# Kernel tuning notes

Measured on AMD Instinct MI355X. Metric: run time of the kernel, lower is better.

Reference implementation:

```python
import jax, jax.numpy as jnp
import numpy as np

OUT, IN, RANK = 4096, 4096, 512
B, S = 4, 2048


def setup_inputs() -> dict:
    key = jax.random.key(0)
    k_x, k_qa, k_qb, k_sa, k_sb, k_b = jax.random.split(key, 6)
    x = jax.random.normal(k_x, (B, S, IN), dtype=jnp.float32)
    # int8-style symmetric quantized CP factors (stored as int32 for the harness)
    q_a = jax.random.randint(k_qa, (OUT, RANK), -127, 127, dtype=jnp.int32)
    q_b = jax.random.randint(k_qb, (IN, RANK), -127, 127, dtype=jnp.int32)
    scale_a = jax.random.uniform(k_sa, (), dtype=jnp.float32) * 0.01 + 1e-4
    scale_b = jax.random.uniform(k_sb, (), dtype=jnp.float32) * 0.01 + 1e-4
    bias = jax.random.normal(k_b, (OUT,), dtype=jnp.float32)
    return {"x": x, "q_a": q_a, "q_b": q_b, "scale_a": scale_a,
            "scale_b": scale_b, "bias": bias}


def reference(x, q_a, q_b, scale_a, scale_b, bias):
    # dequantize_factors(): symmetric per-factor dequant q * scale
    a = q_a.astype(jnp.float32) * scale_a          # [OUT, RANK]
    b = q_b.astype(jnp.float32) * scale_b          # [IN,  RANK]
    # CP reconstruction: weight = factors[0] @ factors[1].T, viewed as [OUT, IN]
    weight = a @ b.T                               # [OUT, IN] (materialized, as in original)
    # F.linear(x, weight, bias) = x @ weight.T + bias
    return jnp.einsum('bsi,oi->bso', x, weight) + bias
```

## Files before the change

kernel.cpp:

```cpp
#include <hip/hip_runtime.h>
#include <hip/hip_fp16.h>


#define M_TOT 8192
#define N_OUT 4096
#define K_IN  4096
#define RANK  512

typedef _Float16 f16x8 __attribute__((ext_vector_type(8)));
typedef float f32x4 __attribute__((ext_vector_type(4)));

#define WAIT_VM0() asm volatile("s_waitcnt vmcnt(0)" ::: "memory")
#define WAIT_VM4() asm volatile("s_waitcnt vmcnt(4)" ::: "memory")
#define WAIT_VM8() asm volatile("s_waitcnt vmcnt(8)" ::: "memory")
#define BARRIER() do { __builtin_amdgcn_s_barrier(); __builtin_amdgcn_sched_barrier(0); } while (0)

__device__ __forceinline__ void gload_lds16(const void* g, void* l) {
  __builtin_amdgcn_global_load_lds(
      (const __attribute__((address_space(1))) unsigned int*)g,
      (__attribute__((address_space(3))) unsigned int*)l, 16, 0, 0);
}

__global__ void k_transpose_qb(const int* __restrict__ qb, __half* __restrict__ qbt) {
  __shared__ __half tile[32][33];
  int tx = threadIdx.x & 31, ty = threadIdx.x >> 5;
  int k0 = blockIdx.x * 32, r0 = blockIdx.y * 32;
#pragma unroll
  for (int j = 0; j < 4; ++j)
    tile[ty + j * 8][tx] = __float2half_rn((float)qb[(size_t)(k0 + ty + j * 8) * RANK + r0 + tx]);
  __syncthreads();
#pragma unroll
  for (int j = 0; j < 4; ++j)
    qbt[(size_t)(r0 + ty + j * 8) * K_IN + k0 + tx] = tile[tx][ty + j * 8];
}

__global__ __launch_bounds__(512, 4) void k_gemm1v(
    const float* __restrict__ X, const __half* __restrict__ Bt,
    __half* __restrict__ P) {
  __shared__ __align__(16) uint4 lds[2][2048];
  const int tid = threadIdx.x;
  const int lane = tid & 63, wid = tid >> 6;
  const int wm = wid & 1, wn = wid >> 1;
  const int blk = blockIdx.x;
  const int xcd = blk & 7, m_t = blk >> 3;
  const int z = xcd >> 1, n_t = xcd & 1;
  const int m0 = m_t * 128, n0 = n_t * 256;
  const int kbeg = z * (K_IN / 4);
  const int fr = lane & 15, fq = lane >> 4;

  f32x4 acc[4][4] = {};

  auto stage = [&](int kt, int buf) {
#pragma unroll
    for (int c = 0; c < 2; ++c) {
      int d = tid + 512 * c;
      int r = d >> 3, s = (d & 7) ^ (r & 7);
      gload_lds16(X + (size_t)(m0 + r) * K_IN + kbeg + kt * 32 + s * 4, &lds[buf][d]);
    }
#pragma unroll
    for (int c = 0; c < 2; ++c) {
      int d = tid + 512 * c;
      int p = d >> 3, u = (d & 7) ^ (p & 7);
      gload_lds16(Bt + (size_t)(n0 + 2 * p + (u >> 2)) * K_IN + kbeg + kt * 32 + (u & 3) * 8,
                  &lds[buf][1024 + d]);
    }
  };

  stage(0, 0);
  stage(1, 1);
  WAIT_VM4();
  BARRIER();

  const int NT = (K_IN / 4) / 32;
  for (int t = 0; t < NT; ++t) {
    const uint4* Ab = &lds[t & 1][0];
    const uint4* Bb = &lds[t & 1][1024];
    f16x8 a[4], b[4];
#pragma unroll
    for (int mi = 0; mi < 4; ++mi) {
      int r = wm * 64 + mi * 16 + fr;
      f32x4 u0 = *(const f32x4*)&Ab[r * 8 + ((fq * 2) ^ (r & 7))];
      f32x4 u1 = *(const f32x4*)&Ab[r * 8 + ((fq * 2 + 1) ^ (r & 7))];
      union { __half2 h[4]; f16x8 v; } pa;
      pa.h[0] = __floats2half2_rn(u0[0], u0[1]);
      pa.h[1] = __floats2half2_rn(u0[2], u0[3]);
      pa.h[2] = __floats2half2_rn(u1[0], u1[1]);
      pa.h[3] = __floats2half2_rn(u1[2], u1[3]);
      a[mi] = pa.v;
    }
#pragma unroll
    for (int ni = 0; ni < 4; ++ni) {
      int r = wn * 64 + ni * 16 + fr;
      int p = r >> 1;
      b[ni] = *(const f16x8*)&Bb[p * 8 + ((((r & 1) << 2) | fq) ^ (p & 7))];
    }
#pragma unroll
    for (int mi = 0; mi < 4; ++mi)
#pragma unroll
      for (int ni = 0; ni < 4; ++ni)
        acc[mi][ni] = __builtin_amdgcn_mfma_f32_16x16x32_f16(a[mi], b[ni], acc[mi][ni], 0, 0, 0);

    if (t == NT - 1) break;
    BARRIER();
    if (t + 2 < NT) {
      stage(t + 2, t & 1);
      WAIT_VM4();
    } else {
      WAIT_VM0();
    }
    BARRIER();
  }

  __half* Pz = P + (size_t)z * M_TOT * RANK;
#pragma unroll
  for (int mi = 0; mi < 4; ++mi)
#pragma unroll
    for (int ni = 0; ni < 4; ++ni) {
      int col = n0 + wn * 64 + ni * 16 + fr;
      int rbase = m0 + wm * 64 + mi * 16 + fq * 4;
#pragma unroll
      for (int j = 0; j < 4; ++j)
        Pz[(size_t)(rbase + j) * RANK + col] = __float2half_rn(acc[mi][ni][j]);
    }
}

__global__ void k_reduce_cvt(const uint4* __restrict__ P, uint4* __restrict__ T8, int n8,
                             const int4* __restrict__ qa, ushort4* __restrict__ qh, int nq4) {
  int b = blockIdx.x;
  int nred = n8 / 256;
  if (b < nred) {
    int i = b * 256 + threadIdx.x;
    float2 f[4] = {};
#pragma unroll
    for (int zz = 0; zz < 4; ++zz) {
      uint4 v = P[(size_t)zz * n8 + i];
      const __half2* h = (const __half2*)&v;
#pragma unroll
      for (int j = 0; j < 4; ++j) {
        float2 g = __half22float2(h[j]);
        f[j].x += g.x; f[j].y += g.y;
      }
    }
    uint4 r;
    __half2* o = (__half2*)&r;
#pragma unroll
    for (int j = 0; j < 4; ++j) o[j] = __floats2half2_rn(f[j].x, f[j].y);
    T8[i] = r;
  } else {
    int i = (b - nred) * 256 + threadIdx.x;
    if (i >= nq4) return;
    int4 v = qa[i];
    ushort4 r;
    r.x = __half_as_ushort(__float2half_rn((float)v.x));
    r.y = __half_as_ushort(__float2half_rn((float)v.y));
    r.z = __half_as_ushort(__float2half_rn((float)v.z));
    r.w = __half_as_ushort(__float2half_rn((float)v.w));
    qh[i] = r;
  }
}

__global__ __launch_bounds__(256, 2) void k_gemm2(
    const __half* __restrict__ T, const __half* __restrict__ QA,
    const float* __restrict__ sa, const float* __restrict__ sb,
    const float* __restrict__ bias, float* __restrict__ Out) {
  __shared__ __align__(16) uint4 lds[2][2048];
  const int tid = threadIdx.x;
  const int lane = tid & 63, wid = tid >> 6, wm = wid & 1, wn = wid >> 1;
  const int flat = blockIdx.x;
  const int xcd = flat & 7, local = flat >> 3;
  const int n_t = xcd * 4 + (local & 3);
  const int m_t = local >> 2;
  const int m0 = m_t * 128, n0 = n_t * 128;
  const int fr = lane & 15, fq = lane >> 4;

  f32x4 acc[4][4] = {};

  auto stage = [&](int kt, int buf) {
#pragma unroll
    for (int c = 0; c < 4; ++c) {
      int d = tid + 256 * c;
      int r = d >> 3, s = (d & 7) ^ (r & 7);
      gload_lds16(T + (size_t)(m0 + r) * RANK + kt * 64 + s * 8, &lds[buf][d]);
    }
#pragma unroll
    for (int c = 0; c < 4; ++c) {
      int d = tid + 256 * c;
      int r = d >> 3, s = (d & 7) ^ (r & 7);
      gload_lds16(QA + (size_t)(n0 + r) * RANK + kt * 64 + s * 8, &lds[buf][1024 + d]);
    }
  };

  stage(0, 0);
  stage(1, 1);
  WAIT_VM8();
  BARRIER();

  const int NT = RANK / 64;
  for (int t = 0; t < NT; ++t) {
    const int cur = t & 1;
#pragma unroll
    for (int kk = 0; kk < 2; ++kk) {
      int s = kk * 4 + fq;
      f16x8 a[4], b[4];
#pragma unroll
      for (int mi = 0; mi < 4; ++mi) {
        int r = wm * 64 + mi * 16 + fr;
        a[mi] = *(const f16x8*)&lds[cur][r * 8 + (s ^ (r & 7))];
      }
#pragma unroll
      for (int ni = 0; ni < 4; ++ni) {
        int n = wn * 64 + ni * 16 + fr;
        b[ni] = *(const f16x8*)&lds[cur][1024 + n * 8 + (s ^ (n & 7))];
      }
#pragma unroll
      for (int mi = 0; mi < 4; ++mi)
#pragma unroll
        for (int ni = 0; ni < 4; ++ni)
          acc[mi][ni] = __builtin_amdgcn_mfma_f32_16x16x32_f16(a[mi], b[ni], acc[mi][ni], 0, 0, 0);
    }
    if (t == NT - 1) break;
    BARRIER();
    if (t + 2 < NT) {
      stage(t + 2, cur);
      WAIT_VM8();
    } else {
      WAIT_VM0();
    }
    BARRIER();
  }

  const float scale = sa[0] * sb[0];
#pragma unroll
  for (int mi = 0; mi < 4; ++mi)
#pragma unroll
    for (int ni = 0; ni < 4; ++ni) {
      int col = n0 + wn * 64 + ni * 16 + fr;
      float bv = bias[col];
      int rbase = m0 + wm * 64 + mi * 16 + fq * 4;
#pragma unroll
      for (int j = 0; j < 4; ++j)
        Out[(size_t)(rbase + j) * N_OUT + col] = acc[mi][ni][j] * scale + bv;
    }
}

extern "C" void kernel_launch(void* const* d_in, const int* in_sizes, int n_in,
                              void* d_out, int out_size, void* d_ws, size_t ws_size,
                              hipStream_t stream) {
  const float* x    = (const float*)d_in[0];
  const int*   qa   = (const int*)d_in[1];
  const int*   qb   = (const int*)d_in[2];
  const float* sa   = (const float*)d_in[3];
  const float* sb   = (const float*)d_in[4];
  const float* bias = (const float*)d_in[5];
  float* out = (float*)d_out;

  char* ws = (char*)d_ws;
  __half* qa_h = (__half*)ws;
  __half* qbt  = (__half*)(ws + (4u << 20));
  __half* t    = (__half*)(ws + (8u << 20));
  __half* part = (__half*)(ws + (16u << 20));

  dim3 tg(K_IN / 32, RANK / 32);
  k_transpose_qb<<<tg, 256, 0, stream>>>(qb, qbt);

  k_gemm1v<<<512, 512, 0, stream>>>(x, qbt, part);

  const int n8 = M_TOT * RANK / 8;
  const int nq4 = N_OUT * RANK / 4;
  const int nred = n8 / 256;
  const int ncvt = (nq4 + 255) / 256;
  k_reduce_cvt<<<nred + ncvt, 256, 0, stream>>>((const uint4*)part, (uint4*)t, n8,
                                                (const int4*)qa, (ushort4*)qa_h, nq4);

  k_gemm2<<<2048, 256, 0, stream>>>(t, qa_h, sa, sb, bias, out);
}
```

Before: 132.3 us.

## Add wide-N split-K=8 GEMM1 variant so each X tile is read once

Adds a first-GEMM kernel in which each block covers the full rank dimension (256 columns per wave-group pair) and splits K eight ways, so each tile of X is loaded and converted to fp16 only once instead of once per N half. The reduce kernel is templated on the split count and sums eight partials. The new path is chosen only when the workspace is at least 80 MB. In exchange it drops the double buffering (single LDS buffer with sync barriers), doubles the accumulator registers, lowers occupancy to 2 blocks, and doubles the partial-sum traffic.

```diff
diff --git a/kernel.cpp b/kernel.cpp
--- a/kernel.cpp
+++ b/kernel.cpp
@@ -32,6 +32,78 @@
 #pragma unroll
   for (int j = 0; j < 4; ++j)
     qbt[(size_t)(r0 + ty + j * 8) * K_IN + k0 + tx] = tile[tx][ty + j * 8];
+}
+
+__global__ __launch_bounds__(512, 2) void k_gemm1w(
+    const float* __restrict__ X, const __half* __restrict__ Bt,
+    __half* __restrict__ P) {
+  __shared__ __align__(16) uint4 lds[3072];
+  const int tid = threadIdx.x;
+  const int lane = tid & 63, wid = tid >> 6;
+  const int wm = wid & 1, wn = wid >> 1;
+  const int blk = blockIdx.x;
+  const int z = blk & 7, m_t = blk >> 3;
+  const int m0 = m_t * 128;
+  const int kbeg = z * (K_IN / 8);
+  const int fr = lane & 15, fq = lane >> 4;
+
+  f32x4 acc[4][8] = {};
+
+  const int NT = (K_IN / 8) / 32;
+  for (int t = 0; t < NT; ++t) {
+    const int k0 = kbeg + t * 32;
+#pragma unroll
+    for (int c = 0; c < 2; ++c) {
+      int d = tid + 512 * c;
+      int r = d >> 3, s = (d & 7) ^ (r & 7);
+      gload_lds16(X + (size_t)(m0 + r) * K_IN + k0 + s * 4, &lds[d]);
+    }
+#pragma unroll
+    for (int c = 0; c < 4; ++c) {
+      int d = tid + 512 * c;
+      int p = d >> 3, u = (d & 7) ^ (p & 7);
+      gload_lds16(Bt + (size_t)(2 * p + (u >> 2)) * K_IN + k0 + (u & 3) * 8,
+                  &lds[1024 + d]);
+    }
+    __syncthreads();
+    f16x8 a[4], b[8];
+#pragma unroll
+    for (int mi = 0; mi < 4; ++mi) {
+      int r = wm * 64 + mi * 16 + fr;
+      f32x4 u0 = *(const f32x4*)&lds[r * 8 + ((fq * 2) ^ (r & 7))];
+      f32x4 u1 = *(const f32x4*)&lds[r * 8 + ((fq * 2 + 1) ^ (r & 7))];
+      union { __half2 h[4]; f16x8 v; } pa;
+      pa.h[0] = __floats2half2_rn(u0[0], u0[1]);
+      pa.h[1] = __floats2half2_rn(u0[2], u0[3]);
+      pa.h[2] = __floats2half2_rn(u1[0], u1[1]);
+      pa.h[3] = __floats2half2_rn(u1[2], u1[3]);
+      a[mi] = pa.v;
+    }
+#pragma unroll
+    for (int ni = 0; ni < 8; ++ni) {
+      int r = wn * 128 + ni * 16 + fr;
+      int p = r >> 1;
+      b[ni] = *(const f16x8*)&lds[1024 + p * 8 + ((((r & 1) << 2) | fq) ^ (p & 7))];
+    }
+#pragma unroll
+    for (int mi = 0; mi < 4; ++mi)
+#pragma unroll
+      for (int ni = 0; ni < 8; ++ni)
+        acc[mi][ni] = __builtin_amdgcn_mfma_f32_16x16x32_f16(a[mi], b[ni], acc[mi][ni], 0, 0, 0);
+    __syncthreads();
+  }
+
+  __half* Pz = P + (size_t)z * M_TOT * RANK;
+#pragma unroll
+  for (int mi = 0; mi < 4; ++mi)
+#pragma unroll
+    for (int ni = 0; ni < 8; ++ni) {
+      int col = wn * 128 + ni * 16 + fr;
+      int rbase = m0 + wm * 64 + mi * 16 + fq * 4;
+#pragma unroll
+      for (int j = 0; j < 4; ++j)
+        Pz[(size_t)(rbase + j) * RANK + col] = __float2half_rn(acc[mi][ni][j]);
+    }
 }
 
 __global__ __launch_bounds__(512, 4) void k_gemm1v(
@@ -124,6 +196,7 @@
     }
 }
 
+template <int SK>
 __global__ void k_reduce_cvt(const uint4* __restrict__ P, uint4* __restrict__ T8, int n8,
                              const int4* __restrict__ qa, ushort4* __restrict__ qh, int nq4) {
   int b = blockIdx.x;
@@ -132,7 +205,7 @@
     int i = b * 256 + threadIdx.x;
     float2 f[4] = {};
 #pragma unroll
-    for (int zz = 0; zz < 4; ++zz) {
+    for (int zz = 0; zz < SK; ++zz) {
       uint4 v = P[(size_t)zz * n8 + i];
       const __half2* h = (const __half2*)&v;
 #pragma unroll
@@ -263,14 +336,20 @@
   dim3 tg(K_IN / 32, RANK / 32);
   k_transpose_qb<<<tg, 256, 0, stream>>>(qb, qbt);
 
-  k_gemm1v<<<512, 512, 0, stream>>>(x, qbt, part);
-
   const int n8 = M_TOT * RANK / 8;
   const int nq4 = N_OUT * RANK / 4;
   const int nred = n8 / 256;
   const int ncvt = (nq4 + 255) / 256;
-  k_reduce_cvt<<<nred + ncvt, 256, 0, stream>>>((const uint4*)part, (uint4*)t, n8,
-                                                (const int4*)qa, (ushort4*)qa_h, nq4);
+
+  if (ws_size >= (80ull << 20)) {
+    k_gemm1w<<<512, 512, 0, stream>>>(x, qbt, part);
+    k_reduce_cvt<8><<<nred + ncvt, 256, 0, stream>>>((const uint4*)part, (uint4*)t, n8,
+                                                     (const int4*)qa, (ushort4*)qa_h, nq4);
+  } else {
+    k_gemm1v<<<512, 512, 0, stream>>>(x, qbt, part);
+    k_reduce_cvt<4><<<nred + ncvt, 256, 0, stream>>>((const uint4*)part, (uint4*)t, n8,
+                                                     (const int4*)qa, (ushort4*)qa_h, nq4);
+  }
 
   k_gemm2<<<2048, 256, 0, stream>>>(t, qa_h, sa, sb, bias, out);
 }
```

After: 154.3 us. +16.7%, slower.
